# Performance work log

Hardware: AMD Instinct MI355X
Metric: run time of the kernel (lower is better)

Reference implementation:

```python
import jax, jax.numpy as jnp
import numpy as np

B, S, H = 2, 1024, 2048
NH, HD = 16, 128
L = 4  # num_prev_layers == attention_window


def _rope(x):
    # x: [..., S, D]; standard rotate-half RoPE, base 10000
    d = x.shape[-1]
    s = x.shape[-2]
    inv_freq = 1.0 / (10000.0 ** (jnp.arange(0, d, 2, dtype=jnp.float32) / d))
    freqs = jnp.outer(jnp.arange(s, dtype=jnp.float32), inv_freq)  # [S, d/2]
    cos, sin = jnp.cos(freqs), jnp.sin(freqs)
    x1, x2 = jnp.split(x, 2, axis=-1)
    return jnp.concatenate([x1 * cos - x2 * sin, x2 * cos + x1 * sin], axis=-1)


def setup_inputs() -> dict:
    key = jax.random.key(0)
    ks = jax.random.split(key, 8)
    std = 0.02
    return {
        "hidden_states": jax.random.normal(ks[0], (B, S, H), jnp.float32),
        "prev_hidden_states": jax.random.normal(ks[1], (L, B, S, H), jnp.float32),
        "Wq": jax.random.normal(ks[2], (H, NH * HD), jnp.float32) * std,
        "bq": jnp.zeros((NH * HD,), jnp.float32),
        "Wk": jax.random.normal(ks[3], (H, NH * HD), jnp.float32) * std,
        "bk": jnp.zeros((NH * HD,), jnp.float32),
        "Wv": jax.random.normal(ks[4], (H, NH * HD), jnp.float32) * std,
        "bv": jnp.zeros((NH * HD,), jnp.float32),
        "Wo": jax.random.normal(ks[5], (NH * HD, H), jnp.float32) * std,
        "bo": jnp.zeros((H,), jnp.float32),
        "Wg": jax.random.normal(ks[6], (H, L), jnp.float32) * std,
    }


def reference(hidden_states, prev_hidden_states, Wq, bq, Wk, bk, Wv, bv, Wo, bo, Wg):
    b, s, _ = hidden_states.shape
    # queries from current layer: [b, nh, s, hd], RoPE applied
    q = (hidden_states @ Wq + bq).reshape(b, s, NH, HD).transpose(0, 2, 1, 3)
    q = _rope(q)
    # keys/values from each prev layer: [L, b, nh, s, hd]
    k = (prev_hidden_states @ Wk + bk).reshape(L, b, s, NH, HD).transpose(0, 1, 3, 2, 4)
    k = _rope(k)
    v = (prev_hidden_states @ Wv + bv).reshape(L, b, s, NH, HD).transpose(0, 1, 3, 2, 4)
    # per-prev-layer attention (no mask)
    scores = jnp.einsum('bhqd,lbhkd->lbhqk', q, k) / jnp.sqrt(jnp.float32(HD))
    attn = jax.nn.softmax(scores, axis=-1)
    lo = jnp.einsum('lbhqk,lbhkd->lbhqd', attn, v)
    lo = lo.transpose(0, 1, 3, 2, 4).reshape(L, b, s, NH * HD)  # merge heads
    # softmax gate over pooled queries -> combine layer outputs
    layer_w = jax.nn.softmax(jnp.mean(hidden_states, axis=1) @ Wg, axis=-1)  # [b, L]
    out = jnp.einsum('lbsh,bl->bsh', lo, layer_w)
    return out @ Wo + bo
```

## Files before the change

kernel.cpp:

```cpp
#include <hip/hip_runtime.h>
#include <hip/hip_bf16.h>
#include <math.h>


typedef __bf16 bf16;
typedef __bf16 bf16x4v __attribute__((ext_vector_type(4)));
typedef __bf16 bf16x8 __attribute__((ext_vector_type(8)));
typedef float f32x4 __attribute__((ext_vector_type(4)));

#define DEV static __device__ __forceinline__

DEV void gload_lds16(const void* g, void* s) {
  __builtin_amdgcn_global_load_lds(
      (const __attribute__((address_space(1))) void*)g,
      (__attribute__((address_space(3))) void*)s, 16, 0, 0);
}

DEV f32x4 mfma16(bf16x8 a, bf16x8 b, f32x4 c) {
  return __builtin_amdgcn_mfma_f32_16x16x32_bf16(a, b, c, 0, 0, 0);
}

__global__ __launch_bounds__(256) void cvt_kernel(const float* __restrict__ in,
                                                  bf16* __restrict__ out, int n4) {
  int i = blockIdx.x * 256 + threadIdx.x;
  if (i >= n4) return;
  const float4 v = ((const float4*)in)[i];
  bf16x4v o;
  o.x = (bf16)v.x; o.y = (bf16)v.y; o.z = (bf16)v.z; o.w = (bf16)v.w;
  ((bf16x4v*)out)[i] = o;
}

__global__ __launch_bounds__(256) void twt_kernel(const float* __restrict__ W,
                                                  bf16* __restrict__ Wt) {
  __shared__ float tile[64][65];
  const int t = threadIdx.x;
  const int n0 = blockIdx.x * 64, k0 = blockIdx.y * 64;
#pragma unroll
  for (int ph = 0; ph < 16; ++ph) {
    int idx = ph * 256 + t, r = idx >> 6, c = idx & 63;
    tile[r][c] = W[(size_t)(k0 + r) * 2048 + n0 + c];
  }
  __syncthreads();
#pragma unroll
  for (int ph = 0; ph < 16; ++ph) {
    int idx = ph * 256 + t, r = idx >> 6, c = idx & 63;
    Wt[(size_t)(n0 + r) * 2048 + k0 + c] = (bf16)tile[c][r];
  }
}

__global__ __launch_bounds__(64) void rope_table_kernel(float* __restrict__ cosT,
                                                        float* __restrict__ sinT) {
  int s = blockIdx.x, j = threadIdx.x;
  float inv = powf(10000.0f, -(float)j * (1.0f / 64.0f));
  float a = (float)s * inv;
  cosT[s * 64 + j] = cosf(a);
  sinT[s * 64 + j] = sinf(a);
}

__global__ __launch_bounds__(256) void rope_kernel(const bf16* __restrict__ raw,
                                                   const float* __restrict__ cosT,
                                                   const float* __restrict__ sinT,
                                                   bf16* __restrict__ outp) {
  int rid = blockIdx.x * 16 + (threadIdx.x >> 4);
  int j = threadIdx.x & 15;
  int s = rid & 1023;
  const bf16* src = raw + (size_t)rid * 128 + 4 * j;
  bf16* dst = outp + (size_t)rid * 128 + 4 * j;
  bf16x4v x1 = *(const bf16x4v*)src;
  bf16x4v x2 = *(const bf16x4v*)(src + 64);
  f32x4 c = *(const f32x4*)(cosT + s * 64 + 4 * j);
  f32x4 sn = *(const f32x4*)(sinT + s * 64 + 4 * j);
  bf16x4v o1, o2;
#pragma unroll
  for (int k = 0; k < 4; ++k) {
    float a = (float)x1[k], b2 = (float)x2[k];
    o1[k] = (bf16)(a * c[k] - b2 * sn[k]);
    o2[k] = (bf16)(b2 * c[k] + a * sn[k]);
  }
  *(bf16x4v*)dst = o1;
  *(bf16x4v*)(dst + 64) = o2;
}

__global__ __launch_bounds__(256) void mean_part_kernel(const float* __restrict__ hs,
                                                        float* __restrict__ part) {
  int bc = blockIdx.x;
  int b = bc >> 3, c0 = (bc & 7) * 256;
  int ss = blockIdx.y;
  int col = c0 + threadIdx.x;
  float s = 0.f;
  for (int r = 0; r < 128; ++r)
    s += hs[((size_t)b * 1024 + ss * 128 + r) * 2048 + col];
  part[(size_t)ss * 4096 + b * 2048 + col] = s;
}

__global__ __launch_bounds__(256) void mean_fin_kernel(const float* __restrict__ part,
                                                       float* __restrict__ meanb) {
  int c = blockIdx.x * 256 + threadIdx.x;
  float s = 0.f;
#pragma unroll
  for (int j = 0; j < 8; ++j) s += part[(size_t)j * 4096 + c];
  meanb[c] = s * (1.0f / 1024.0f);
}

__global__ __launch_bounds__(256) void gate_kernel(const float* __restrict__ meanb,
                                                   const float* __restrict__ Wg,
                                                   float* __restrict__ lwout) {
  __shared__ float red[8][256];
  int t = threadIdx.x;
  float p[8];
#pragma unroll
  for (int j = 0; j < 8; ++j) p[j] = 0.f;
  for (int hh = t; hh < 2048; hh += 256) {
    float m0 = meanb[hh], m1 = meanb[2048 + hh];
#pragma unroll
    for (int ll = 0; ll < 4; ++ll) {
      float g = Wg[hh * 4 + ll];
      p[ll] += m0 * g;
      p[4 + ll] += m1 * g;
    }
  }
#pragma unroll
  for (int j = 0; j < 8; ++j) red[j][t] = p[j];
  __syncthreads();
  for (int s2 = 128; s2 > 0; s2 >>= 1) {
    if (t < s2) {
#pragma unroll
      for (int j = 0; j < 8; ++j) red[j][t] += red[j][t + s2];
    }
    __syncthreads();
  }
  if (t == 0) {
#pragma unroll
    for (int bb = 0; bb < 2; ++bb) {
      float v0 = red[bb * 4 + 0][0], v1 = red[bb * 4 + 1][0];
      float v2 = red[bb * 4 + 2][0], v3 = red[bb * 4 + 3][0];
      float mx = fmaxf(fmaxf(v0, v1), fmaxf(v2, v3));
      float e0 = __expf(v0 - mx), e1 = __expf(v1 - mx);
      float e2 = __expf(v2 - mx), e3 = __expf(v3 - mx);
      float inv = 1.0f / (e0 + e1 + e2 + e3);
      lwout[bb * 4 + 0] = e0 * inv;
      lwout[bb * 4 + 1] = e1 * inv;
      lwout[bb * 4 + 2] = e2 * inv;
      lwout[bb * 4 + 3] = e3 * inv;
    }
  }
}

template <int OUTMODE>
__global__ __launch_bounds__(256) void gemm_kernel(const bf16* __restrict__ A,
                                                   const bf16* __restrict__ Bt,
                                                   const float* __restrict__ bias,
                                                   void* __restrict__ Cout,
                                                   int M, int N, int K) {
  __shared__ __attribute__((aligned(16))) bf16 As[2][128 * 64];
  __shared__ __attribute__((aligned(16))) bf16 Bs[2][128 * 64];
  const int t = threadIdx.x;
  const int w = t >> 6, l = t & 63;
  const int lo = l & 15, hi = l >> 4;
  const int wr = w >> 1, wc = w & 1;

  const int nwg = gridDim.x * gridDim.y;
  int flat = blockIdx.y * gridDim.x + blockIdx.x;
  int swz = (flat & 7) * (nwg >> 3) + (flat >> 3);
  const int bx = swz % gridDim.x, by = swz / gridDim.x;

  f32x4 acc[4][4];
#pragma unroll
  for (int m = 0; m < 4; ++m)
#pragma unroll
    for (int n = 0; n < 4; ++n)
#pragma unroll
      for (int q = 0; q < 4; ++q) acc[m][n][q] = 0.f;

  int srow[4], scl[4];
#pragma unroll
  for (int p = 0; p < 4; ++p) {
    int id = p * 256 + t;
    int r = id >> 3, cph = id & 7;
    srow[p] = r;
    scl[p] = cph ^ (r & 7);
  }

  const bf16* Ab = A + (size_t)by * 128 * K;
  const bf16* Bb = Bt + (size_t)bx * 128 * K;

  auto stage = [&](int bi, int kt) {
#pragma unroll
    for (int p = 0; p < 4; ++p)
      gload_lds16(Ab + (size_t)srow[p] * K + kt + scl[p] * 8,
                  &As[bi][(p * 256 + w * 64) * 8]);
#pragma unroll
    for (int p = 0; p < 4; ++p)
      gload_lds16(Bb + (size_t)srow[p] * K + kt + scl[p] * 8,
                  &Bs[bi][(p * 256 + w * 64) * 8]);
  };

  stage(0, 0);
  int cur = 0;
  for (int kt = 0; kt < K; kt += 64) {
    if (kt + 64 < K) {
      stage(cur ^ 1, kt + 64);
      asm volatile("s_waitcnt vmcnt(8)" ::: "memory");
    } else {
      asm volatile("s_waitcnt vmcnt(0)" ::: "memory");
    }
    __builtin_amdgcn_s_barrier();
    __builtin_amdgcn_sched_barrier(0);
    __builtin_amdgcn_s_setprio(1);
#pragma unroll
    for (int ks = 0; ks < 2; ++ks) {
      bf16x8 af[4], bfr[4];
#pragma unroll
      for (int m = 0; m < 4; ++m) {
        int row = wr * 64 + m * 16 + lo;
        int ch = (ks * 4 + hi) ^ (row & 7);
        af[m] = *(const bf16x8*)&As[cur][row * 64 + ch * 8];
      }
#pragma unroll
      for (int n = 0; n < 4; ++n) {
        int row = wc * 64 + n * 16 + lo;
        int ch = (ks * 4 + hi) ^ (row & 7);
        bfr[n] = *(const bf16x8*)&Bs[cur][row * 64 + ch * 8];
      }
#pragma unroll
      for (int m = 0; m < 4; ++m)
#pragma unroll
        for (int n = 0; n < 4; ++n)
          acc[m][n] = mfma16(af[m], bfr[n], acc[m][n]);
    }
    __builtin_amdgcn_s_setprio(0);
    __builtin_amdgcn_s_barrier();
    cur ^= 1;
  }

  if (OUTMODE == 2) {
#pragma unroll
    for (int m = 0; m < 4; ++m) {
#pragma unroll
      for (int i = 0; i < 4; ++i) {
        size_t row = (size_t)by * 128 + wr * 64 + m * 16 + hi * 4 + i;
        float rb = bias[row];
#pragma unroll
        for (int n = 0; n < 4; ++n) {
          int col = bx * 128 + wc * 64 + n * 16 + lo;
          int pos64 = ((n >> 1) << 5) + ((lo >> 2) << 3) + ((n & 1) << 2) + (lo & 3);
          int colp = (col & ~63) | pos64;
          float v = acc[m][n][i] + rb;
          ((bf16*)Cout)[(size_t)(colp >> 10) * 2097152 + row * 1024 + (colp & 1023)] =
              (bf16)v;
        }
      }
    }
  } else {
#pragma unroll
    for (int n = 0; n < 4; ++n) {
      int col = bx * 128 + wc * 64 + n * 16 + lo;
      float bb = bias[col];
#pragma unroll
      for (int m = 0; m < 4; ++m) {
#pragma unroll
        for (int i = 0; i < 4; ++i) {
          size_t row = (size_t)by * 128 + wr * 64 + m * 16 + hi * 4 + i;
          float v = acc[m][n][i] + bb;
          if (OUTMODE == 1)
            ((float*)Cout)[row * N + col] = v;
          else if (OUTMODE == 0)
            ((bf16*)Cout)[row * N + col] = (bf16)v;
          else {
            size_t g = (row >> 10) * 16 + (col >> 7);
            ((bf16*)Cout)[(g * 1024 + (row & 1023)) * 128 + (col & 127)] = (bf16)v;
          }
        }
      }
    }
  }
}

__global__ __launch_bounds__(256, 2) void attn_kernel(const bf16* __restrict__ Q,
                                                      const bf16* __restrict__ Kb,
                                                      const bf16* __restrict__ Vt,
                                                      const float* __restrict__ lw,
                                                      bf16* __restrict__ Obuf) {
  __shared__ __attribute__((aligned(16))) bf16 Ks[2][64 * 128];
  __shared__ __attribute__((aligned(16))) bf16 Vs[2][128 * 64];
  const int t = threadIdx.x, w = t >> 6, l = t & 63;
  const int lo = l & 15, hi = l >> 4;
  const int bh = blockIdx.x;
  const int qt = blockIdx.y;
  const int li = blockIdx.z;
  const int b = bh >> 4, h = bh & 15;
  const float C2 = 0.08838834764831845f * 1.44269504f;
  const float M2 = 64.0f * C2;

  bf16x8 qf[2][4];
#pragma unroll
  for (int qs = 0; qs < 2; ++qs) {
    const bf16* qptr =
        Q + ((size_t)bh * 1024 + qt * 128 + w * 32 + qs * 16 + lo) * 128;
#pragma unroll
    for (int db = 0; db < 4; ++db)
      qf[qs][db] = *(const bf16x8*)(qptr + db * 32 + hi * 8);
  }

  int krow[4], kcl[4], vrow[4], vcl[4];
#pragma unroll
  for (int p = 0; p < 4; ++p) {
    int id = p * 256 + t;
    krow[p] = id >> 4;
    kcl[p] = (id & 15) ^ (krow[p] & 7);
    vrow[p] = id >> 3;
    vcl[p] = (id & 7) ^ (vrow[p] & 7);
  }

  const bf16* Kl = Kb + ((size_t)li * 32 + bh) * (size_t)131072;
  const bf16* Vl = Vt + ((size_t)li * 32 + bh) * (size_t)131072;

  float si0 = 0.f, si1 = 0.f;
  f32x4 oacc[2][8];
#pragma unroll
  for (int qs = 0; qs < 2; ++qs)
#pragma unroll
    for (int dc = 0; dc < 8; ++dc)
#pragma unroll
      for (int q = 0; q < 4; ++q) oacc[qs][dc][q] = 0.f;

  auto stage = [&](int bi, int kt2) {
    const bf16* Ksrc = Kl + (size_t)kt2 * 8192;
#pragma unroll
    for (int p = 0; p < 4; ++p)
      gload_lds16(Ksrc + (size_t)krow[p] * 128 + kcl[p] * 8,
                  &Ks[bi][(p * 256 + w * 64) * 8]);
#pragma unroll
    for (int p = 0; p < 4; ++p)
      gload_lds16(Vl + (size_t)vrow[p] * 1024 + kt2 * 64 + vcl[p] * 8,
                  &Vs[bi][(p * 256 + w * 64) * 8]);
  };

  auto softmax_step = [&](f32x4 (&sa)[4], float& si, bf16x8 (&pf2)[2]) {
    float rs = 0.f;
    bf16x4v pk[4];
#pragma unroll
    for (int kc = 0; kc < 4; ++kc) {
#pragma unroll
      for (int i = 0; i < 4; ++i) {
        float pf_ = __builtin_amdgcn_exp2f(fmaf(sa[kc][i], C2, -M2));
        rs += pf_;
        pk[kc][i] = (bf16)pf_;
      }
    }
    rs += __shfl_xor(rs, 16);
    rs += __shfl_xor(rs, 32);
    si += rs;
    pf2[0] = __builtin_shufflevector(pk[0], pk[1], 0, 1, 2, 3, 4, 5, 6, 7);
    pf2[1] = __builtin_shufflevector(pk[2], pk[3], 0, 1, 2, 3, 4, 5, 6, 7);
  };

  stage(0, 0);
  int cur = 0;
  for (int kt = 0; kt < 16; ++kt) {
    if (kt < 15) {
      stage(cur ^ 1, kt + 1);
      asm volatile("s_waitcnt vmcnt(8)" ::: "memory");
    } else {
      asm volatile("s_waitcnt vmcnt(0)" ::: "memory");
    }
    __builtin_amdgcn_s_barrier();
    __builtin_amdgcn_sched_barrier(0);

    f32x4 sa[2][4];
#pragma unroll
    for (int qs = 0; qs < 2; ++qs)
#pragma unroll
      for (int kc = 0; kc < 4; ++kc)
#pragma unroll
        for (int q = 0; q < 4; ++q) sa[qs][kc][q] = 0.f;
    __builtin_amdgcn_s_setprio(1);
#pragma unroll
    for (int kc = 0; kc < 4; ++kc) {
      int row = kc * 16 + lo;
#pragma unroll
      for (int db = 0; db < 4; ++db) {
        int ch = (db * 4 + hi) ^ (row & 7);
        bf16x8 kf = *(const bf16x8*)&Ks[cur][row * 128 + ch * 8];
        sa[0][kc] = mfma16(kf, qf[0][db], sa[0][kc]);
        sa[1][kc] = mfma16(kf, qf[1][db], sa[1][kc]);
      }
    }
    __builtin_amdgcn_s_setprio(0);

    bf16x8 pfr[2][2];
    softmax_step(sa[0], si0, pfr[0]);
    softmax_step(sa[1], si1, pfr[1]);

    __builtin_amdgcn_s_setprio(1);
#pragma unroll
    for (int kvc = 0; kvc < 2; ++kvc) {
#pragma unroll
      for (int dc = 0; dc < 8; ++dc) {
        int rowv = dc * 16 + lo;
        int ch = (kvc * 4 + hi) ^ (rowv & 7);
        bf16x8 vf = *(const bf16x8*)&Vs[cur][rowv * 64 + ch * 8];
        oacc[0][dc] = mfma16(pfr[0][kvc], vf, oacc[0][dc]);
        oacc[1][dc] = mfma16(pfr[1][kvc], vf, oacc[1][dc]);
      }
    }
    __builtin_amdgcn_s_setprio(0);
    __builtin_amdgcn_s_barrier();
    cur ^= 1;
  }

  float wl = lw[b * 4 + li];
#pragma unroll
  for (int qs = 0; qs < 2; ++qs) {
    float sv = (qs == 0) ? si0 : si1;
    float inv[4];
#pragma unroll
    for (int i = 0; i < 4; ++i) inv[i] = wl / __shfl(sv, hi * 4 + i);
#pragma unroll
    for (int dc = 0; dc < 8; ++dc) {
      int col = h * 128 + dc * 16 + lo;
#pragma unroll
      for (int i = 0; i < 4; ++i) {
        int srow = qt * 128 + w * 32 + qs * 16 + hi * 4 + i;
        Obuf[((size_t)(li * 2 + b) * 1024 + srow) * 2048 + col] =
            (bf16)(oacc[qs][dc][i] * inv[i]);
      }
    }
  }
}

__global__ __launch_bounds__(256) void comb_kernel(const bf16* __restrict__ Obuf,
                                                   bf16* __restrict__ comb) {
  size_t i = ((size_t)blockIdx.x * 256 + threadIdx.x) * 8;
  bf16x8 a0 = *(const bf16x8*)(Obuf + i);
  bf16x8 a1 = *(const bf16x8*)(Obuf + 4194304 + i);
  bf16x8 a2 = *(const bf16x8*)(Obuf + 8388608 + i);
  bf16x8 a3 = *(const bf16x8*)(Obuf + 12582912 + i);
  bf16x8 o;
#pragma unroll
  for (int j = 0; j < 8; ++j)
    o[j] = (bf16)((float)a0[j] + (float)a1[j] + (float)a2[j] + (float)a3[j]);
  *(bf16x8*)(comb + i) = o;
}

extern "C" void kernel_launch(void* const* d_in, const int* in_sizes, int n_in,
                              void* d_out, int out_size, void* d_ws, size_t ws_size,
                              hipStream_t stream) {
  (void)in_sizes; (void)n_in; (void)out_size; (void)ws_size;
  const float* hs = (const float*)d_in[0];
  const float* prev = (const float*)d_in[1];
  const float* Wq = (const float*)d_in[2];
  const float* bq = (const float*)d_in[3];
  const float* Wk = (const float*)d_in[4];
  const float* bk = (const float*)d_in[5];
  const float* Wv = (const float*)d_in[6];
  const float* bv = (const float*)d_in[7];
  const float* Wo = (const float*)d_in[8];
  const float* bo = (const float*)d_in[9];
  const float* Wg = (const float*)d_in[10];
  float* out = (float*)d_out;

  char* ws = (char*)d_ws;
  bf16* hs_bf = (bf16*)(ws + 0);
  bf16* prev_bf = (bf16*)(ws + 8388608);
  bf16* WqT = (bf16*)(ws + 41943040);
  bf16* WkT = (bf16*)(ws + 50331648);
  bf16* WvT = (bf16*)(ws + 58720256);
  bf16* Qraw2 = (bf16*)(ws + 67108864);
  bf16* WoT = (bf16*)(ws + 75497472);
  bf16* Kraw2 = (bf16*)(ws + 83886080);
  bf16* Vt = (bf16*)(ws + 117440512);
  float* cosT = (float*)(ws + 150994944);
  float* sinT = (float*)(ws + 151257088);
  float* part = (float*)(ws + 151519232);
  float* meanb = (float*)(ws + 151650304);
  float* lwbuf = (float*)(ws + 151666688);
  bf16* Qbf = hs_bf;
  bf16* Kbf = prev_bf;
  bf16* Obuf = Kraw2;
  bf16* comb = (bf16*)(ws + 0);

  cvt_kernel<<<4096, 256, 0, stream>>>(hs, hs_bf, 2048 * 2048 / 4);
  cvt_kernel<<<16384, 256, 0, stream>>>(prev, prev_bf, 8192 * 2048 / 4);

  twt_kernel<<<dim3(32, 32), 256, 0, stream>>>(Wq, WqT);
  twt_kernel<<<dim3(32, 32), 256, 0, stream>>>(Wk, WkT);
  twt_kernel<<<dim3(32, 32), 256, 0, stream>>>(Wv, WvT);
  twt_kernel<<<dim3(32, 32), 256, 0, stream>>>(Wo, WoT);

  rope_table_kernel<<<1024, 64, 0, stream>>>(cosT, sinT);
  mean_part_kernel<<<dim3(16, 8), 256, 0, stream>>>(hs, part);
  mean_fin_kernel<<<16, 256, 0, stream>>>(part, meanb);
  gate_kernel<<<1, 256, 0, stream>>>(meanb, Wg, lwbuf);

  gemm_kernel<3><<<dim3(16, 16), 256, 0, stream>>>(hs_bf, WqT, bq, Qraw2, 2048, 2048, 2048);
  gemm_kernel<3><<<dim3(16, 64), 256, 0, stream>>>(prev_bf, WkT, bk, Kraw2, 8192, 2048, 2048);
  gemm_kernel<2><<<dim3(64, 16), 256, 0, stream>>>(WvT, prev_bf, bv, Vt, 2048, 8192, 2048);

  rope_kernel<<<2048, 256, 0, stream>>>(Qraw2, cosT, sinT, Qbf);
  rope_kernel<<<8192, 256, 0, stream>>>(Kraw2, cosT, sinT, Kbf);

  attn_kernel<<<dim3(32, 8, 4), 256, 0, stream>>>(Qbf, Kbf, Vt, lwbuf, Obuf);

  comb_kernel<<<2048, 256, 0, stream>>>(Obuf, comb);

  gemm_kernel<1><<<dim3(16, 16), 256, 0, stream>>>(comb, WoT, bo, out, 2048, 2048, 2048);
}
```

Baseline: 394.0 us.

## Fuse K and V projection GEMMs into one kernel with 256x256 tiles

```diff
diff --git a/kernel.cpp b/kernel.cpp
--- a/kernel.cpp
+++ b/kernel.cpp
@@ -233,43 +233,147 @@
     cur ^= 1;
   }
 
-  if (OUTMODE == 2) {
+#pragma unroll
+  for (int n = 0; n < 4; ++n) {
+    int col = bx * 128 + wc * 64 + n * 16 + lo;
+    float bb = bias[col];
 #pragma unroll
     for (int m = 0; m < 4; ++m) {
 #pragma unroll
       for (int i = 0; i < 4; ++i) {
         size_t row = (size_t)by * 128 + wr * 64 + m * 16 + hi * 4 + i;
-        float rb = bias[row];
+        float v = acc[m][n][i] + bb;
+        if (OUTMODE == 1)
+          ((float*)Cout)[row * N + col] = v;
+        else if (OUTMODE == 0)
+          ((bf16*)Cout)[row * N + col] = (bf16)v;
+        else {
+          size_t g = (row >> 10) * 16 + (col >> 7);
+          ((bf16*)Cout)[(g * 1024 + (row & 1023)) * 128 + (col & 127)] = (bf16)v;
+        }
+      }
+    }
+  }
+}
+
+__global__ __launch_bounds__(512, 4) void gemm_kv_kernel(
+    const bf16* __restrict__ prev, const bf16* __restrict__ WkT,
+    const bf16* __restrict__ WvT, const float* __restrict__ bk,
+    const float* __restrict__ bv, bf16* __restrict__ Kout,
+    bf16* __restrict__ Vout) {
+  __shared__ __attribute__((aligned(16))) bf16 As[2][8192];
+  __shared__ __attribute__((aligned(16))) bf16 Bs[2][8192];
+  const int t = threadIdx.x;
+  const int w = t >> 6, l = t & 63;
+  const int lo = l & 15, hi = l >> 4;
+  const int wm = w >> 2, wn = w & 3;
+
+  const int bid = blockIdx.x;
+  const int grp = bid >> 8;
+  const int sub = bid & 255;
+  const int swz = (sub & 7) * 32 + (sub >> 3);
+  const int mt = (grp == 0) ? (swz >> 3) : (swz & 7);
+  const int nt = (grp == 0) ? (swz & 7) : (swz >> 3);
+  const bf16* Ab = ((grp == 0) ? prev : WvT) + (size_t)mt * 256 * 2048;
+  const bf16* Bb = ((grp == 0) ? WkT : prev) + (size_t)nt * 256 * 2048;
+
+  f32x4 acc[8][4];
+#pragma unroll
+  for (int m = 0; m < 8; ++m)
+#pragma unroll
+    for (int n = 0; n < 4; ++n)
+#pragma unroll
+      for (int q = 0; q < 4; ++q) acc[m][n][q] = 0.f;
+
+  int srow[2], skk[2];
+#pragma unroll
+  for (int p = 0; p < 2; ++p) {
+    int id = p * 512 + t;
+    int line = id >> 3;
+    int sg = (id & 7) ^ (line & 7);
+    srow[p] = line * 2 + (sg >> 2);
+    skk[p] = (sg & 3) << 3;
+  }
+
+  auto stage = [&](int bi, int kt) {
+#pragma unroll
+    for (int p = 0; p < 2; ++p)
+      gload_lds16(Ab + (size_t)srow[p] * 2048 + kt + skk[p],
+                  &As[bi][(p * 512 + w * 64) * 8]);
+#pragma unroll
+    for (int p = 0; p < 2; ++p)
+      gload_lds16(Bb + (size_t)srow[p] * 2048 + kt + skk[p],
+                  &Bs[bi][(p * 512 + w * 64) * 8]);
+  };
+
+  stage(0, 0);
+  int cur = 0;
+  for (int kt = 0; kt < 2048; kt += 32) {
+    if (kt + 32 < 2048) {
+      stage(cur ^ 1, kt + 32);
+      asm volatile("s_waitcnt vmcnt(4)" ::: "memory");
+    } else {
+      asm volatile("s_waitcnt vmcnt(0)" ::: "memory");
+    }
+    __builtin_amdgcn_s_barrier();
+    __builtin_amdgcn_sched_barrier(0);
+    __builtin_amdgcn_s_setprio(1);
+    bf16x8 af[8], bfr[4];
+#pragma unroll
+    for (int m = 0; m < 8; ++m) {
+      int r = wm * 128 + m * 16 + lo;
+      int line = r >> 1;
+      int s = (((r & 1) << 2) | hi) ^ (line & 7);
+      af[m] = *(const bf16x8*)&As[cur][line * 64 + s * 8];
+    }
+#pragma unroll
+    for (int n = 0; n < 4; ++n) {
+      int r = wn * 64 + n * 16 + lo;
+      int line = r >> 1;
+      int s = (((r & 1) << 2) | hi) ^ (line & 7);
+      bfr[n] = *(const bf16x8*)&Bs[cur][line * 64 + s * 8];
+    }
+#pragma unroll
+    for (int m = 0; m < 8; ++m)
+#pragma unroll
+      for (int n = 0; n < 4; ++n)
+        acc[m][n] = mfma16(af[m], bfr[n], acc[m][n]);
+    __builtin_amdgcn_s_setprio(0);
+    __builtin_amdgcn_s_barrier();
+    cur ^= 1;
+  }
+
+  if (grp == 0) {
+#pragma unroll
+    for (int n = 0; n < 4; ++n) {
+      int col = nt * 256 + wn * 64 + n * 16 + lo;
+      float bb = bk[col];
+#pragma unroll
+      for (int m = 0; m < 8; ++m) {
+#pragma unroll
+        for (int i = 0; i < 4; ++i) {
+          size_t row = (size_t)mt * 256 + wm * 128 + m * 16 + hi * 4 + i;
+          float v = acc[m][n][i] + bb;
+          size_t g = (row >> 10) * 16 + (col >> 7);
+          Kout[(g * 1024 + (row & 1023)) * 128 + (col & 127)] = (bf16)v;
+        }
+      }
+    }
+  } else {
+#pragma unroll
+    for (int m = 0; m < 8; ++m) {
+#pragma unroll
+      for (int i = 0; i < 4; ++i) {
+        size_t row = (size_t)mt * 256 + wm * 128 + m * 16 + hi * 4 + i;
+        float rb = bv[row];
 #pragma unroll
         for (int n = 0; n < 4; ++n) {
-          int col = bx * 128 + wc * 64 + n * 16 + lo;
+          int col = nt * 256 + wn * 64 + n * 16 + lo;
           int pos64 = ((n >> 1) << 5) + ((lo >> 2) << 3) + ((n & 1) << 2) + (lo & 3);
           int colp = (col & ~63) | pos64;
           float v = acc[m][n][i] + rb;
-          ((bf16*)Cout)[(size_t)(colp >> 10) * 2097152 + row * 1024 + (colp & 1023)] =
+          Vout[(size_t)(colp >> 10) * 2097152 + row * 1024 + (colp & 1023)] =
               (bf16)v;
-        }
-      }
-    }
-  } else {
-#pragma unroll
-    for (int n = 0; n < 4; ++n) {
-      int col = bx * 128 + wc * 64 + n * 16 + lo;
-      float bb = bias[col];
-#pragma unroll
-      for (int m = 0; m < 4; ++m) {
-#pragma unroll
-        for (int i = 0; i < 4; ++i) {
-          size_t row = (size_t)by * 128 + wr * 64 + m * 16 + hi * 4 + i;
-          float v = acc[m][n][i] + bb;
-          if (OUTMODE == 1)
-            ((float*)Cout)[row * N + col] = v;
-          else if (OUTMODE == 0)
-            ((bf16*)Cout)[row * N + col] = (bf16)v;
-          else {
-            size_t g = (row >> 10) * 16 + (col >> 7);
-            ((bf16*)Cout)[(g * 1024 + (row & 1023)) * 128 + (col & 127)] = (bf16)v;
-          }
         }
       }
     }
@@ -494,8 +598,7 @@
   gate_kernel<<<1, 256, 0, stream>>>(meanb, Wg, lwbuf);
 
   gemm_kernel<3><<<dim3(16, 16), 256, 0, stream>>>(hs_bf, WqT, bq, Qraw2, 2048, 2048, 2048);
-  gemm_kernel<3><<<dim3(16, 64), 256, 0, stream>>>(prev_bf, WkT, bk, Kraw2, 8192, 2048, 2048);
-  gemm_kernel<2><<<dim3(64, 16), 256, 0, stream>>>(WvT, prev_bf, bv, Vt, 2048, 8192, 2048);
+  gemm_kv_kernel<<<512, 512, 0, stream>>>(prev_bf, WkT, WvT, bk, bv, Kraw2, Vt);
 
   rope_kernel<<<2048, 256, 0, stream>>>(Qraw2, cosT, sinT, Qbf);
   rope_kernel<<<8192, 256, 0, stream>>>(Kraw2, cosT, sinT, Kbf);
```

After: 1.245 ms. 3.16x slower.
